# Performance work log

Hardware: AMD Instinct MI355X
Metric: run time of the kernel (lower is better)

Reference implementation:

```python
import jax, jax.numpy as jnp
import numpy as np

B, T1, CHUNK = 4, 512, 64
LEFT, RIGHT = 256, 64
T2 = T1 + LEFT + RIGHT          # 832
NPOS = 2 * T1 - 1 + LEFT + RIGHT  # 1343
NFEAT, H, DK = 1024, 16, 64


def setup_inputs() -> dict:
    key = jax.random.key(0)
    ks = jax.random.split(key, 14)
    s = 0.02
    inp = {
        "query":   jax.random.normal(ks[0], (B, T1, NFEAT), jnp.float32),
        "key":     jax.random.normal(ks[1], (B, T2, NFEAT), jnp.float32),
        "value":   jax.random.normal(ks[2], (B, T2, NFEAT), jnp.float32),
        "pos_emb": jax.random.normal(ks[3], (1, NPOS, NFEAT), jnp.float32),
        "Wq":   jax.random.normal(ks[4], (NFEAT, NFEAT), jnp.float32) * s,
        "bq":   jax.random.normal(ks[5], (NFEAT,), jnp.float32) * s,
        "Wk":   jax.random.normal(ks[6], (NFEAT, NFEAT), jnp.float32) * s,
        "bk":   jax.random.normal(ks[7], (NFEAT,), jnp.float32) * s,
        "Wv":   jax.random.normal(ks[8], (NFEAT, NFEAT), jnp.float32) * s,
        "bv":   jax.random.normal(ks[9], (NFEAT,), jnp.float32) * s,
        "Wpos": jax.random.normal(ks[10], (NFEAT, NFEAT), jnp.float32) * s,
        "Wout": jax.random.normal(ks[11], (NFEAT, NFEAT), jnp.float32) * s,
        "bout": jax.random.normal(ks[12], (NFEAT,), jnp.float32) * s,
        "pos_bias_u": jax.random.normal(ks[13], (H, DK), jnp.float32) * s,
        "pos_bias_v": jax.random.normal(jax.random.fold_in(key, 99), (H, DK), jnp.float32) * s,
    }
    # chunk mask with right context: key index j maps to absolute position a = j - LEFT;
    # query i (chunk c = i // CHUNK) may attend a in [c*CHUNK - LEFT, (c+1)*CHUNK + RIGHT)
    c = np.arange(T1) // CHUNK
    a = np.arange(T2) - LEFT
    allowed = (a[None, :] < (c[:, None] + 1) * CHUNK + RIGHT) & (a[None, :] >= c[:, None] * CHUNK - LEFT)
    inp["mask"] = jnp.broadcast_to(jnp.asarray(allowed, dtype=bool)[None], (B, T1, T2))
    inp["left_context_size"] = LEFT
    inp["right_context_size"] = RIGHT
    return inp


def _rel_shift(x, left, right):
    # x: (b, h, t1, 2*t1-1+left+right) -> (b, h, t1, t1+left+right)
    # matches torch as_strided: out[..., i, j] = x[..., i, j - i + t1 - 1]
    b, h, t1, n = x.shape
    t2 = t1 + left + right
    idx = jnp.arange(t2)[None, :] - jnp.arange(t1)[:, None] + (t1 - 1)  # (t1, t2)
    return jnp.take_along_axis(x, idx[None, None], axis=-1)


def reference(query, key, value, pos_emb, mask, Wq, bq, Wk, bk, Wv, bv,
              Wpos, Wout, bout, pos_bias_u, pos_bias_v,
              left_context_size, right_context_size):
    b, t1, _ = query.shape
    q = (query @ Wq.T + bq).reshape(b, t1, H, DK)                       # (b, t1, h, d)
    k = (key @ Wk.T + bk).reshape(b, -1, H, DK).transpose(0, 2, 1, 3)    # (b, h, t2, d)
    v = (value @ Wv.T + bv).reshape(b, -1, H, DK).transpose(0, 2, 1, 3)  # (b, h, t2, d)
    p = (pos_emb @ Wpos.T).reshape(pos_emb.shape[0], -1, H, DK).transpose(0, 2, 1, 3)  # (1, h, n, d)

    q_u = (q + pos_bias_u).transpose(0, 2, 1, 3)   # (b, h, t1, d)
    q_v = (q + pos_bias_v).transpose(0, 2, 1, 3)   # (b, h, t1, d)

    matrix_ac = jnp.einsum('bhqd,bhkd->bhqk', q_u, k)          # (b, h, t1, t2)
    matrix_bd = jnp.einsum('bhqd,ohnd->bhqn', q_v, p)          # (b, h, t1, n)
    matrix_bd = _rel_shift(matrix_bd, left_context_size, right_context_size)

    scores = (matrix_ac + matrix_bd) / jnp.sqrt(jnp.float32(DK))
    m = mask[:, None, :, :]                                    # (b, 1, t1, t2), True = attend
    scores = jnp.where(m, scores, -jnp.inf)
    attn = jax.nn.softmax(scores.astype(jnp.float32), axis=-1).astype(value.dtype)
    attn = jnp.where(m, attn, 0.0)

    x = jnp.einsum('bhqk,bhkd->bqhd', attn, v).reshape(b, t1, H * DK)
    out = x @ Wout.T + bout                                     # (b, t1, n_feat)
    new_cache = jnp.concatenate([k, v], axis=-1)                # (b, h, t2, 2*d)
    return out, new_cache
```

## Files before the change

kernel.cpp:

```cpp
#include <hip/hip_runtime.h>
#include <cstdint>

typedef unsigned short u16;
using short8 = __attribute__((ext_vector_type(8))) short;
using f32x4  = __attribute__((ext_vector_type(4))) float;

#define T1 512
#define T2 832
#define NH 16
#define NPLOC 448

__device__ __forceinline__ u16 f2b(float f){
  union { float f; uint32_t u; } c; c.f = f;
  uint32_t u = c.u;
  u += 0x7fffu + ((u >> 16) & 1u);
  return (u16)(u >> 16);
}
__device__ __forceinline__ float b2f(u16 b){
  union { uint32_t u; float f; } c; c.u = (uint32_t)b << 16; return c.f;
}
__device__ __forceinline__ void async16(const void* g, void* l){
  __builtin_amdgcn_global_load_lds(
      (const __attribute__((address_space(1))) unsigned int*)g,
      (__attribute__((address_space(3))) unsigned int*)l, 16, 0, 0);
}

#define SB0 __builtin_amdgcn_sched_barrier(0)

struct CvtSeg { const float* src; u16* dst; int nblk; };
struct CvtArgs { CvtSeg s[9]; };

__global__ __launch_bounds__(256) void cvt_all(CvtArgs a){
  int rel = blockIdx.x, seg = 0;
  while (rel >= a.s[seg].nblk){ rel -= a.s[seg].nblk; ++seg; }
  int i = rel * 256 + threadIdx.x;
  float4 v = ((const float4*)a.s[seg].src)[i];
  uint64_t p = (uint64_t)f2b(v.x) | ((uint64_t)f2b(v.y) << 16)
             | ((uint64_t)f2b(v.z) << 32) | ((uint64_t)f2b(v.w) << 48);
  *(uint64_t*)(a.s[seg].dst + (size_t)i * 4) = p;
}

struct G4Args {
  const u16 *q, *k, *v, *p;
  const u16 *Wq, *Wk, *Wv, *Wp;
  const float *bq, *bk, *bv, *pbu, *pbv;
  u16 *qu, *qv2, *katt, *vatt, *patt;
  float *cache;
};

__global__ __launch_bounds__(256, 2) void gemm4(G4Args ga){
  __shared__ __align__(16) u16 As0[8192];
  __shared__ __align__(16) u16 As1[8192];
  __shared__ __align__(16) u16 Bs0[8192];
  __shared__ __align__(16) u16 Bs1[8192];

  int bid0 = blockIdx.x;
  int bid = (bid0 & 7) * 72 + (bid0 >> 3);
  int tid = threadIdx.x;
  int mode, mb; const u16 *A, *W;
  if (bid < 128)      { mode = 0; mb = bid >> 3;         A = ga.q; W = ga.Wq; }
  else if (bid < 336) { mode = 1; mb = (bid - 128) >> 3; A = ga.k; W = ga.Wk; }
  else if (bid < 544) { mode = 2; mb = (bid - 336) >> 3; A = ga.v; W = ga.Wv; }
  else                { mode = 3; mb = (bid - 544) >> 3; A = ga.p; W = ga.Wp; }
  int m0 = mb * 128, n0 = (bid & 7) * 128;

  int lane = tid & 63, w = tid >> 6;
  int wr = w >> 1, wc = w & 1;
  const int lr = lane & 15, g = lane >> 4;
  const int r7 = lr & 7;

  int srow = tid >> 3;
  int ssl = ((tid & 7) ^ (srow & 7)) * 8;
  const u16* Asrc = A + (size_t)(m0 + srow) * 1024 + ssl;
  const u16* Bsrc = W + (size_t)(n0 + srow) * 1024 + ssl;

  f32x4 acc[4][4] = {};

  auto stage = [&](int k0, u16* as, u16* bs){
    #pragma unroll
    for (int cc = 0; cc < 4; ++cc){
      async16(Asrc + (size_t)cc*32768 + k0, as + cc*2048 + tid*8);
      async16(Bsrc + (size_t)cc*32768 + k0, bs + cc*2048 + tid*8);
    }
  };

  auto step = [&](u16* as, u16* bs, int kstage, bool do_stage, bool last){
    if (last) asm volatile("s_waitcnt vmcnt(0)" ::: "memory");
    else      asm volatile("s_waitcnt vmcnt(8)" ::: "memory");
    SB0; __builtin_amdgcn_s_barrier(); SB0;
    short8 a[2][4], b[2][4];
    #pragma unroll
    for (int kk = 0; kk < 2; ++kk){
      int sl = ((kk*4 + g) ^ r7) * 8;
      #pragma unroll
      for (int m = 0; m < 4; ++m) a[kk][m] = *(const short8*)&as[(wr*64 + m*16 + lr)*64 + sl];
      #pragma unroll
      for (int n = 0; n < 4; ++n) b[kk][n] = *(const short8*)&bs[(wc*64 + n*16 + lr)*64 + sl];
    }
    asm volatile("s_waitcnt lgkmcnt(0)" ::: "memory");
    SB0; __builtin_amdgcn_s_barrier(); SB0;
    if (do_stage) stage(kstage, as, bs);
    SB0;
    __builtin_amdgcn_s_setprio(1);
    #pragma unroll
    for (int kk = 0; kk < 2; ++kk)
      #pragma unroll
      for (int m = 0; m < 4; ++m)
        #pragma unroll
        for (int n = 0; n < 4; ++n)
          acc[m][n] = __builtin_amdgcn_mfma_f32_16x16x32_bf16(a[kk][m], b[kk][n], acc[m][n], 0, 0, 0);
    __builtin_amdgcn_s_setprio(0);
  };

  stage(0,  As0, Bs0);
  stage(64, As1, Bs1);
  SB0;
  for (int it = 0; it < 8; ++it){
    step(As0, Bs0, it*128 + 128, it < 7, false);
    step(As1, Bs1, it*128 + 192, it < 7, it == 7);
  }

  #pragma unroll
  for (int m = 0; m < 4; ++m){
    #pragma unroll
    for (int n = 0; n < 4; ++n){
      #pragma unroll
      for (int j = 0; j < 4; ++j){
        int row = m0 + wr*64 + m*16 + g*4 + j;
        int col = n0 + wc*64 + n*16 + lr;
        float vv = acc[m][n][j];
        if (mode == 0){
          vv += ga.bq[col];
          int h = col >> 6, d = col & 63, b_ = row >> 9, t = row & 511;
          size_t o = ((size_t)((b_*NH + h)*T1 + t))*64 + d;
          ga.qu [o] = f2b(vv + ga.pbu[col]);
          ga.qv2[o] = f2b(vv + ga.pbv[col]);
        } else if (mode == 1 || mode == 2){
          vv += (mode == 1 ? ga.bk : ga.bv)[col];
          int h = col >> 6, d = col & 63;
          int b_ = row / T2, t2 = row - b_*T2;
          size_t base = (size_t)(b_*NH + h)*T2 + t2;
          ga.cache[base*128 + (mode == 2 ? 64 : 0) + d] = vv;
          (mode == 1 ? ga.katt : ga.vatt)[base*64 + d] = f2b(vv);
        } else {
          if (row < NPLOC){
            int h = col >> 6, d = col & 63;
            ga.patt[((size_t)h*NPLOC + row)*64 + d] = f2b(vv);
          }
        }
      }
    }
  }
}

__device__ __forceinline__ void gemm_core64(const u16* __restrict__ A, const u16* __restrict__ W,
    int m0, int n0, int tid, f32x4 acc[4][2])
{
  __shared__ __align__(16) u16 As0[2048];
  __shared__ __align__(16) u16 As1[2048];
  __shared__ __align__(16) u16 Bs0[4096];
  __shared__ __align__(16) u16 Bs1[4096];

  int lane = tid & 63, wc = tid >> 6;
  const int lr = lane & 15, g = lane >> 4;
  const int sslot = (g ^ ((lr >> 1) & 3)) * 8;

  int r = tid >> 2;
  int ssl = ((tid & 3) ^ ((tid >> 3) & 3)) * 8;
  const u16* Asrc = A + (size_t)(m0 + r) * 1024 + ssl;
  const u16* Bsrc = W + (size_t)(n0 + r) * 1024 + ssl;

  auto stage = [&](int k0, u16* as, u16* bs){
    async16(Asrc + k0,         as + tid*8);
    async16(Bsrc + k0,         bs + tid*8);
    async16(Bsrc + 65536 + k0, bs + 2048 + tid*8);
  };

  auto step = [&](u16* as, u16* bs, int kstage, bool do_stage, bool last){
    if (last) asm volatile("s_waitcnt vmcnt(0)" ::: "memory");
    else      asm volatile("s_waitcnt vmcnt(3)" ::: "memory");
    SB0; __builtin_amdgcn_s_barrier(); SB0;
    short8 a[4], b[2];
    #pragma unroll
    for (int m = 0; m < 4; ++m) a[m] = *(const short8*)&as[(m*16 + lr)*32 + sslot];
    #pragma unroll
    for (int n = 0; n < 2; ++n) b[n] = *(const short8*)&bs[(wc*32 + n*16 + lr)*32 + sslot];
    asm volatile("s_waitcnt lgkmcnt(0)" ::: "memory");
    SB0; __builtin_amdgcn_s_barrier(); SB0;
    if (do_stage) stage(kstage, as, bs);
    SB0;
    __builtin_amdgcn_s_setprio(1);
    #pragma unroll
    for (int m = 0; m < 4; ++m)
      #pragma unroll
      for (int n = 0; n < 2; ++n)
        acc[m][n] = __builtin_amdgcn_mfma_f32_16x16x32_bf16(a[m], b[n], acc[m][n], 0, 0, 0);
    __builtin_amdgcn_s_setprio(0);
  };

  stage(0,  As0, Bs0);
  stage(32, As1, Bs1);
  SB0;
  for (int it = 0; it < 16; ++it){
    step(As0, Bs0, it*64 + 64, it < 15, false);
    step(As1, Bs1, it*64 + 96, it < 15, it == 15);
  }
}

__global__ __launch_bounds__(256, 4) void gemm_out(const u16* __restrict__ A, const u16* __restrict__ W,
                                                   const float* __restrict__ bias, float* __restrict__ out){
  int bid0 = blockIdx.x;
  int bid = (bid0 & 7) * 32 + (bid0 >> 3);
  int m0 = (bid >> 3) * 64, n0 = (bid & 7) * 128;
  int tid = threadIdx.x;
  f32x4 acc[4][2] = {};
  gemm_core64(A, W, m0, n0, tid, acc);
  int lane = tid & 63, wc = tid >> 6;
  const int lr = lane & 15, g = lane >> 4;
  #pragma unroll
  for (int m = 0; m < 4; ++m)
    #pragma unroll
    for (int n = 0; n < 2; ++n)
      #pragma unroll
      for (int j = 0; j < 4; ++j){
        int row = m0 + m*16 + g*4 + j;
        int col = n0 + wc*32 + n*16 + lr;
        out[(size_t)row*1024 + col] = acc[m][n][j] + bias[col];
      }
}

#define PHASE_HEAD(N) \
  asm volatile("s_waitcnt vmcnt(" #N ")" ::: "memory"); \
  SB0; __builtin_amdgcn_s_barrier(); SB0;

#define PHASE_TAIL \
  SB0; __builtin_amdgcn_s_barrier(); SB0;

#define VT_TAIL \
  asm volatile("s_waitcnt lgkmcnt(0)" ::: "memory"); \
  SB0; __builtin_amdgcn_s_barrier(); SB0;

__global__ __launch_bounds__(256, 2) void attn_v3(
    const u16* __restrict__ qu, const u16* __restrict__ qv,
    const u16* __restrict__ katt, const u16* __restrict__ vatt,
    const u16* __restrict__ patt, u16* __restrict__ xout)
{
  __shared__ __align__(16) u16 SB[64*384];
  __shared__ __align__(16) u16 S0[8192];
  __shared__ __align__(16) u16 S1[8192];

  int tid = threadIdx.x, lane = tid & 63, w = tid >> 6;
  int bid0 = blockIdx.x;
  int bid = (bid0 & 7) * 64 + (bid0 >> 3);
  int c = bid & 7, h = (bid >> 3) & 15, b = bid >> 7;
  int bh = b*NH + h;
  const int lr = lane & 15, g = lane >> 4, lk = g * 8;

  auto sb_off = [&](int r, int cc) -> uint32_t {
    return ((uint32_t)(r*384 + cc)*2) ^ ((uint32_t)(r & 15) << 4);
  };
  auto stg_swz = [&](uint32_t o) -> uint32_t { return o ^ (((o >> 7) & 7u) << 4); };
  auto vt_off = [&](int d, int kk) -> uint32_t {
    return ((uint32_t)(d*128 + kk)*2) ^ ((uint32_t)(((d & 7) ^ ((d >> 3) & 7))) << 4);
  };

  int qrow = 16*w + lr;
  const u16* qub = qu + ((size_t)bh*T1 + c*64 + qrow)*64;
  const u16* qvb = qv + ((size_t)bh*T1 + c*64 + qrow)*64;
  short8 qu0 = *(const short8*)(qub + lk);
  short8 qu1 = *(const short8*)(qub + 32 + lk);
  short8 qv0 = *(const short8*)(qvb + lk);
  short8 qv1 = *(const short8*)(qvb + 32 + lk);
  SB0;

  const char* psrc = (const char*)(patt + (size_t)h*NPLOC*64);
  const char* ksrc = (const char*)(katt + ((size_t)bh*T2 + c*64)*64);
  const u16*  vsrc = vatt + ((size_t)bh*T2 + c*64)*64;

  auto issue4 = [&](const char* src, u16* dst){
    #pragma unroll
    for (int i = 0; i < 4; ++i){
      uint32_t o = (uint32_t)(i*256 + tid)*16;
      async16(src + stg_swz(o), (char*)dst + o);
    }
  };

  uint4 vstg0, vstg1, vstg2, vstg3;
  auto vload = [&](int vc){
    const u16* vb = vsrc + vc*8192;
    vstg0 = *(const uint4*)(vb + (0*256 + tid)*8);
    vstg1 = *(const uint4*)(vb + (1*256 + tid)*8);
    vstg2 = *(const uint4*)(vb + (2*256 + tid)*8);
    vstg3 = *(const uint4*)(vb + (3*256 + tid)*8);
  };
  auto vtwrite = [&](u16* sbuf){
    #pragma unroll
    for (int i = 0; i < 4; ++i){
      uint4 vv4 = (i == 0) ? vstg0 : (i == 1) ? vstg1 : (i == 2) ? vstg2 : vstg3;
      int e = (i*256 + tid)*8;
      int kk = e >> 6, d0 = e & 63;
      u16 uu[8] = { (u16)(vv4.x & 0xffff), (u16)(vv4.x >> 16), (u16)(vv4.y & 0xffff), (u16)(vv4.y >> 16),
                    (u16)(vv4.z & 0xffff), (u16)(vv4.z >> 16), (u16)(vv4.w & 0xffff), (u16)(vv4.w >> 16) };
      #pragma unroll
      for (int j = 0; j < 8; ++j)
        *(u16*)((char*)sbuf + vt_off(d0 + j, kk)) = uu[j];
    }
  };

  #define BD_CHUNK(PC, SBUF) \
    _Pragma("unroll") \
    for (int nt = 0; nt < 8; ++nt){ \
      uint32_t bo = (uint32_t)((nt*16 + lr)*64)*2; \
      short8 b0 = *(const short8*)((const char*)SBUF + stg_swz(bo + lk*2)); \
      short8 b1 = *(const short8*)((const char*)SBUF + stg_swz(bo + (32 + lk)*2)); \
      f32x4 acc = {0.f,0.f,0.f,0.f}; \
      __builtin_amdgcn_s_setprio(1); \
      acc = __builtin_amdgcn_mfma_f32_16x16x32_bf16(qv0, b0, acc, 0, 0, 0); \
      acc = __builtin_amdgcn_mfma_f32_16x16x32_bf16(qv1, b1, acc, 0, 0, 0); \
      __builtin_amdgcn_s_setprio(0); \
      int nl = (PC)*128 + nt*16 + lr; \
      _Pragma("unroll") \
      for (int j = 0; j < 4; ++j){ \
        int r = 16*w + g*4 + j; \
        int jj = nl + r - 63; \
        if (jj >= 0 && jj < 384) *(u16*)((char*)SB + sb_off(r, jj)) = f2b(acc[j]); \
      } \
    }

  #define AC_CHUNK(KC, SBUF) \
    _Pragma("unroll") \
    for (int nt = 0; nt < 8; ++nt){ \
      uint32_t bo = (uint32_t)((nt*16 + lr)*64)*2; \
      short8 b0 = *(const short8*)((const char*)SBUF + stg_swz(bo + lk*2)); \
      short8 b1 = *(const short8*)((const char*)SBUF + stg_swz(bo + (32 + lk)*2)); \
      __builtin_amdgcn_s_setprio(1); \
      accs[(KC)*8 + nt] = __builtin_amdgcn_mfma_f32_16x16x32_bf16(qu0, b0, accs[(KC)*8 + nt], 0, 0, 0); \
      accs[(KC)*8 + nt] = __builtin_amdgcn_mfma_f32_16x16x32_bf16(qu1, b1, accs[(KC)*8 + nt], 0, 0, 0); \
      __builtin_amdgcn_s_setprio(0); \
    }

  #define PV_CHUNK(VC, SBUF) \
    _Pragma("unroll") \
    for (int kt = 0; kt < 4; ++kt){ \
      short8 a = *(const short8*)((const char*)SB + sb_off(16*w + lr, (VC)*128 + kt*32 + lk)); \
      __builtin_amdgcn_s_setprio(1); \
      _Pragma("unroll") \
      for (int n = 0; n < 4; ++n){ \
        short8 bb = *(const short8*)((const char*)SBUF + vt_off(n*16 + lr, kt*32 + lk)); \
        acco[n] = __builtin_amdgcn_mfma_f32_16x16x32_bf16(a, bb, acco[n], 0, 0, 0); \
      } \
      __builtin_amdgcn_s_setprio(0); \
    }

  f32x4 accs[24];
  #pragma unroll
  for (int t = 0; t < 24; ++t) accs[t] = (f32x4){0.f,0.f,0.f,0.f};
  f32x4 acco[4] = {};

  issue4(psrc,          S0);
  issue4(psrc + 16384,  S1);

  PHASE_HEAD(4) BD_CHUNK(0, S0) PHASE_TAIL issue4(psrc + 32768, S0);
  PHASE_HEAD(4) BD_CHUNK(1, S1) PHASE_TAIL issue4(psrc + 49152, S1);
  PHASE_HEAD(4) BD_CHUNK(2, S0) PHASE_TAIL issue4(ksrc,         S0);
  PHASE_HEAD(4) BD_CHUNK(3, S1) PHASE_TAIL issue4(ksrc + 16384, S1);
  PHASE_HEAD(4) AC_CHUNK(0, S0) PHASE_TAIL issue4(ksrc + 32768, S0);
  PHASE_HEAD(4) AC_CHUNK(1, S1) PHASE_TAIL vload(0);
  PHASE_HEAD(4) AC_CHUNK(2, S0)

  #pragma unroll
  for (int t = 0; t < 24; ++t)
    #pragma unroll
    for (int j = 0; j < 4; ++j){
      int r = 16*w + g*4 + j, cc = t*16 + lr;
      accs[t][j] += b2f(*(const u16*)((const char*)SB + sb_off(r, cc)));
    }
  float mx[4] = {-1e30f,-1e30f,-1e30f,-1e30f};
  #pragma unroll
  for (int t = 0; t < 24; ++t)
    #pragma unroll
    for (int j = 0; j < 4; ++j) mx[j] = fmaxf(mx[j], accs[t][j]);
  #pragma unroll
  for (int j = 0; j < 4; ++j){
    mx[j] = fmaxf(mx[j], __shfl_xor(mx[j], 1));
    mx[j] = fmaxf(mx[j], __shfl_xor(mx[j], 2));
    mx[j] = fmaxf(mx[j], __shfl_xor(mx[j], 4));
    mx[j] = fmaxf(mx[j], __shfl_xor(mx[j], 8));
  }
  float sm[4] = {0.f,0.f,0.f,0.f};
  #pragma unroll
  for (int t = 0; t < 24; ++t)
    #pragma unroll
    for (int j = 0; j < 4; ++j){
      accs[t][j] = __expf((accs[t][j] - mx[j]) * 0.125f);
      sm[j] += accs[t][j];
    }
  #pragma unroll
  for (int j = 0; j < 4; ++j){
    sm[j] += __shfl_xor(sm[j], 1);
    sm[j] += __shfl_xor(sm[j], 2);
    sm[j] += __shfl_xor(sm[j], 4);
    sm[j] += __shfl_xor(sm[j], 8);
    sm[j] = 1.f / sm[j];
  }
  #pragma unroll
  for (int t = 0; t < 24; ++t)
    #pragma unroll
    for (int j = 0; j < 4; ++j){
      int r = 16*w + g*4 + j, cc = t*16 + lr;
      *(u16*)((char*)SB + sb_off(r, cc)) = f2b(accs[t][j] * sm[j]);
    }

  asm volatile("s_waitcnt vmcnt(0)" ::: "memory");
  SB0;
  vtwrite(S1);
  vload(1);
  VT_TAIL

  PV_CHUNK(0, S1)
  asm volatile("s_waitcnt vmcnt(0)" ::: "memory");
  SB0;
  vtwrite(S0);
  vload(2);
  VT_TAIL

  PV_CHUNK(1, S0)
  asm volatile("s_waitcnt vmcnt(0)" ::: "memory");
  SB0;
  vtwrite(S1);
  VT_TAIL

  PV_CHUNK(2, S1)

  #pragma unroll
  for (int n = 0; n < 4; ++n)
    #pragma unroll
    for (int j = 0; j < 4; ++j){
      int r = 16*w + g*4 + j;
      int t = c*64 + r, d = n*16 + lr;
      xout[((size_t)b*T1 + t)*1024 + h*64 + d] = f2b(acco[n][j]);
    }
}

extern "C" void kernel_launch(void* const* d_in, const int* in_sizes, int n_in,
                              void* d_out, int out_size, void* d_ws, size_t ws_size,
                              hipStream_t stream)
{
  const float* query = (const float*)d_in[0];
  const float* key   = (const float*)d_in[1];
  const float* value = (const float*)d_in[2];
  const float* pos   = (const float*)d_in[3];
  const float* Wq  = (const float*)d_in[4];
  const float* bq  = (const float*)d_in[5];
  const float* Wk  = (const float*)d_in[6];
  const float* bk  = (const float*)d_in[7];
  const float* Wv  = (const float*)d_in[8];
  const float* bv  = (const float*)d_in[9];
  const float* Wp  = (const float*)d_in[10];
  const float* Wo  = (const float*)d_in[11];
  const float* bo  = (const float*)d_in[12];
  const float* pbu = (const float*)d_in[13];
  const float* pbv = (const float*)d_in[14];

  float* out   = (float*)d_out;
  float* cache = out + 2097152;

  u16* ws     = (u16*)d_ws;
  u16* q_bf   = ws;
  u16* key_bf = ws + 2097152;
  u16* val_bf = ws + 5505024;
  u16* pos_bf = ws + 8912896;
  u16* Wq_bf  = ws + 9437184;
  u16* Wk_bf  = ws + 10485760;
  u16* Wv_bf  = ws + 11534336;
  u16* Wp_bf  = ws + 12582912;
  u16* Wo_bf  = ws + 13631488;
  u16* qu_bf  = ws + 14680064;
  u16* qv_bf  = ws + 16777216;
  u16* katt   = ws + 18874368;
  u16* vatt   = ws + 22282240;
  u16* patt   = ws + 25690112;
  u16* x_bf   = ws + 26148864;

  CvtArgs ca;
  ca.s[0] = { query,            q_bf,   2048 };
  ca.s[1] = { key,              key_bf, 3328 };
  ca.s[2] = { value,            val_bf, 3328 };
  ca.s[3] = { Wq,               Wq_bf,  1024 };
  ca.s[4] = { Wk,               Wk_bf,  1024 };
  ca.s[5] = { Wv,               Wv_bf,  1024 };
  ca.s[6] = { Wp,               Wp_bf,  1024 };
  ca.s[7] = { Wo,               Wo_bf,  1024 };
  ca.s[8] = { pos + 448*1024,   pos_bf, 448 };
  cvt_all<<<14272, 256, 0, stream>>>(ca);

  G4Args ga;
  ga.q = q_bf; ga.k = key_bf; ga.v = val_bf; ga.p = pos_bf;
  ga.Wq = Wq_bf; ga.Wk = Wk_bf; ga.Wv = Wv_bf; ga.Wp = Wp_bf;
  ga.bq = bq; ga.bk = bk; ga.bv = bv; ga.pbu = pbu; ga.pbv = pbv;
  ga.qu = qu_bf; ga.qv2 = qv_bf; ga.katt = katt; ga.vatt = vatt; ga.patt = patt;
  ga.cache = cache;
  gemm4<<<576, 256, 0, stream>>>(ga);

  attn_v3<<<512, 256, 0, stream>>>(qu_bf, qv_bf, katt, vatt, patt, x_bf);

  gemm_out<<<256, 256, 0, stream>>>(x_bf, Wo_bf, bo, out);
}
```

Measured before the change: 99.07 us.

## Fuse fp32-to-bf16 activation conversion into projection GEMM A-tile loads

Activations (query, key, value, pos) are no longer pre-converted by cvt_all. The projection GEMM now async-loads fp32 A tiles into LDS and packs them to bf16 in registers just before the MFMAs. This removes a full write and read of the bf16 activation copies. In exchange the K tile shrinks from 64 to 32, so there are twice as many pipeline steps and barriers, and occupancy is raised to 3 blocks to fit the smaller LDS footprint.

```diff
diff --git a/kernel.cpp b/kernel.cpp
--- a/kernel.cpp
+++ b/kernel.cpp
@@ -1,4 +1,5 @@
 #include <hip/hip_runtime.h>
+#include <hip/hip_bf16.h>
 #include <cstdint>
 
 typedef unsigned short u16;
@@ -24,11 +25,21 @@
       (const __attribute__((address_space(1))) unsigned int*)g,
       (__attribute__((address_space(3))) unsigned int*)l, 16, 0, 0);
 }
+__device__ __forceinline__ short8 pk8(float4 fa, float4 fb){
+  union { __hip_bfloat162 h; uint32_t u; } c0, c1, c2, c3;
+  c0.h = __float22bfloat162_rn(make_float2(fa.x, fa.y));
+  c1.h = __float22bfloat162_rn(make_float2(fa.z, fa.w));
+  c2.h = __float22bfloat162_rn(make_float2(fb.x, fb.y));
+  c3.h = __float22bfloat162_rn(make_float2(fb.z, fb.w));
+  union { uint32_t u[4]; short8 s; } r;
+  r.u[0] = c0.u; r.u[1] = c1.u; r.u[2] = c2.u; r.u[3] = c3.u;
+  return r.s;
+}
 
 #define SB0 __builtin_amdgcn_sched_barrier(0)
 
 struct CvtSeg { const float* src; u16* dst; int nblk; };
-struct CvtArgs { CvtSeg s[9]; };
+struct CvtArgs { CvtSeg s[5]; };
 
 __global__ __launch_bounds__(256) void cvt_all(CvtArgs a){
   int rel = blockIdx.x, seg = 0;
@@ -41,23 +52,23 @@
 }
 
 struct G4Args {
-  const u16 *q, *k, *v, *p;
+  const float *q, *k, *v, *p;
   const u16 *Wq, *Wk, *Wv, *Wp;
   const float *bq, *bk, *bv, *pbu, *pbv;
   u16 *qu, *qv2, *katt, *vatt, *patt;
   float *cache;
 };
 
-__global__ __launch_bounds__(256, 2) void gemm4(G4Args ga){
-  __shared__ __align__(16) u16 As0[8192];
-  __shared__ __align__(16) u16 As1[8192];
-  __shared__ __align__(16) u16 Bs0[8192];
-  __shared__ __align__(16) u16 Bs1[8192];
+__global__ __launch_bounds__(256, 3) void gemm4(G4Args ga){
+  __shared__ __align__(16) float As0[4096];
+  __shared__ __align__(16) float As1[4096];
+  __shared__ __align__(16) u16   Bs0[4096];
+  __shared__ __align__(16) u16   Bs1[4096];
 
   int bid0 = blockIdx.x;
   int bid = (bid0 & 7) * 72 + (bid0 >> 3);
   int tid = threadIdx.x;
-  int mode, mb; const u16 *A, *W;
+  int mode, mb; const float *A; const u16 *W;
   if (bid < 128)      { mode = 0; mb = bid >> 3;         A = ga.q; W = ga.Wq; }
   else if (bid < 336) { mode = 1; mb = (bid - 128) >> 3; A = ga.k; W = ga.Wk; }
   else if (bid < 544) { mode = 2; mb = (bid - 336) >> 3; A = ga.v; W = ga.Wv; }
@@ -67,57 +78,60 @@
   int lane = tid & 63, w = tid >> 6;
   int wr = w >> 1, wc = w & 1;
   const int lr = lane & 15, g = lane >> 4;
+  const int sslot = (g ^ ((lr >> 1) & 3)) * 8;
   const int r7 = lr & 7;
 
-  int srow = tid >> 3;
-  int ssl = ((tid & 7) ^ (srow & 7)) * 8;
-  const u16* Asrc = A + (size_t)(m0 + srow) * 1024 + ssl;
-  const u16* Bsrc = W + (size_t)(n0 + srow) * 1024 + ssl;
+  const float* Af = A + (size_t)(m0 + (tid >> 3)) * 1024 + ((tid & 7) ^ ((tid >> 3) & 7)) * 4;
+  const u16* Bsrc = W + (size_t)(n0 + (tid >> 2)) * 1024 + ((tid & 3) ^ ((tid >> 3) & 3)) * 8;
 
   f32x4 acc[4][4] = {};
 
-  auto stage = [&](int k0, u16* as, u16* bs){
-    #pragma unroll
-    for (int cc = 0; cc < 4; ++cc){
-      async16(Asrc + (size_t)cc*32768 + k0, as + cc*2048 + tid*8);
-      async16(Bsrc + (size_t)cc*32768 + k0, bs + cc*2048 + tid*8);
-    }
-  };
-
-  auto step = [&](u16* as, u16* bs, int kstage, bool do_stage, bool last){
+  auto stage = [&](int kt, float* as, u16* bs){
+    #pragma unroll
+    for (int cc = 0; cc < 4; ++cc)
+      async16(Af + kt*32 + cc*32768, (char*)as + cc*4096 + tid*16);
+    async16(Bsrc + kt*32,         bs + tid*8);
+    async16(Bsrc + kt*32 + 65536, bs + 2048 + tid*8);
+  };
+
+  auto step = [&](float* as, u16* bs, int kstage, bool do_stage, bool last){
     if (last) asm volatile("s_waitcnt vmcnt(0)" ::: "memory");
-    else      asm volatile("s_waitcnt vmcnt(8)" ::: "memory");
+    else      asm volatile("s_waitcnt vmcnt(6)" ::: "memory");
     SB0; __builtin_amdgcn_s_barrier(); SB0;
-    short8 a[2][4], b[2][4];
-    #pragma unroll
-    for (int kk = 0; kk < 2; ++kk){
-      int sl = ((kk*4 + g) ^ r7) * 8;
-      #pragma unroll
-      for (int m = 0; m < 4; ++m) a[kk][m] = *(const short8*)&as[(wr*64 + m*16 + lr)*64 + sl];
-      #pragma unroll
-      for (int n = 0; n < 4; ++n) b[kk][n] = *(const short8*)&bs[(wc*64 + n*16 + lr)*64 + sl];
-    }
+    const char* ab = (const char*)as;
+    float4 fa[4], fb[4];
+    short8 b[4];
+    #pragma unroll
+    for (int m = 0; m < 4; ++m){
+      int rr = wr*64 + m*16 + lr;
+      int s0 = (g*2) ^ r7;
+      fa[m] = *(const float4*)(ab + rr*128 + s0*16);
+      fb[m] = *(const float4*)(ab + rr*128 + (s0^1)*16);
+    }
+    #pragma unroll
+    for (int n = 0; n < 4; ++n) b[n] = *(const short8*)&bs[(wc*64 + n*16 + lr)*32 + sslot];
     asm volatile("s_waitcnt lgkmcnt(0)" ::: "memory");
     SB0; __builtin_amdgcn_s_barrier(); SB0;
     if (do_stage) stage(kstage, as, bs);
     SB0;
+    short8 a[4];
+    #pragma unroll
+    for (int m = 0; m < 4; ++m) a[m] = pk8(fa[m], fb[m]);
     __builtin_amdgcn_s_setprio(1);
     #pragma unroll
-    for (int kk = 0; kk < 2; ++kk)
+    for (int m = 0; m < 4; ++m)
       #pragma unroll
-      for (int m = 0; m < 4; ++m)
-        #pragma unroll
-        for (int n = 0; n < 4; ++n)
-          acc[m][n] = __builtin_amdgcn_mfma_f32_16x16x32_bf16(a[kk][m], b[kk][n], acc[m][n], 0, 0, 0);
+      for (int n = 0; n < 4; ++n)
+        acc[m][n] = __builtin_amdgcn_mfma_f32_16x16x32_bf16(a[m], b[n], acc[m][n], 0, 0, 0);
     __builtin_amdgcn_s_setprio(0);
   };
 
-  stage(0,  As0, Bs0);
-  stage(64, As1, Bs1);
+  stage(0, As0, Bs0);
+  stage(1, As1, Bs1);
   SB0;
-  for (int it = 0; it < 8; ++it){
-    step(As0, Bs0, it*128 + 128, it < 7, false);
-    step(As1, Bs1, it*128 + 192, it < 7, it == 7);
+  for (int it = 0; it < 16; ++it){
+    step(As0, Bs0, 2*it + 2, it < 15, false);
+    step(As1, Bs1, 2*it + 3, it < 15, it == 15);
   }
 
   #pragma unroll
@@ -466,10 +480,6 @@
   float* cache = out + 2097152;
 
   u16* ws     = (u16*)d_ws;
-  u16* q_bf   = ws;
-  u16* key_bf = ws + 2097152;
-  u16* val_bf = ws + 5505024;
-  u16* pos_bf = ws + 8912896;
   u16* Wq_bf  = ws + 9437184;
   u16* Wk_bf  = ws + 10485760;
   u16* Wv_bf  = ws + 11534336;
@@ -483,19 +493,15 @@
   u16* x_bf   = ws + 26148864;
 
   CvtArgs ca;
-  ca.s[0] = { query,            q_bf,   2048 };
-  ca.s[1] = { key,              key_bf, 3328 };
-  ca.s[2] = { value,            val_bf, 3328 };
-  ca.s[3] = { Wq,               Wq_bf,  1024 };
-  ca.s[4] = { Wk,               Wk_bf,  1024 };
-  ca.s[5] = { Wv,               Wv_bf,  1024 };
-  ca.s[6] = { Wp,               Wp_bf,  1024 };
-  ca.s[7] = { Wo,               Wo_bf,  1024 };
-  ca.s[8] = { pos + 448*1024,   pos_bf, 448 };
-  cvt_all<<<14272, 256, 0, stream>>>(ca);
+  ca.s[0] = { Wq, Wq_bf, 1024 };
+  ca.s[1] = { Wk, Wk_bf, 1024 };
+  ca.s[2] = { Wv, Wv_bf, 1024 };
+  ca.s[3] = { Wp, Wp_bf, 1024 };
+  ca.s[4] = { Wo, Wo_bf, 1024 };
+  cvt_all<<<5120, 256, 0, stream>>>(ca);
 
   G4Args ga;
-  ga.q = q_bf; ga.k = key_bf; ga.v = val_bf; ga.p = pos_bf;
+  ga.q = query; ga.k = key; ga.v = value; ga.p = pos + 448*1024;
   ga.Wq = Wq_bf; ga.Wk = Wk_bf; ga.Wv = Wv_bf; ga.Wp = Wp_bf;
   ga.bq = bq; ga.bk = bk; ga.bv = bv; ga.pbu = pbu; ga.pbv = pbv;
   ga.qu = qu_bf; ga.qv2 = qv_bf; ga.katt = katt; ga.vatt = vatt; ga.patt = patt;
```

Result: faster. 91.26 us (-7.9%).

## Halve gemm4 K-tile for higher occupancy and move pos-bias add into attention

Applied to the files above, without the earlier changes.

The projection GEMM now stages 32-wide K slices instead of 64-wide, halving shared memory per block so launch bounds can allow 4 blocks per CU. The main loop runs twice as many iterations with half the loads per stage. Separately, the Q projection writes a single bf16 Q tensor, and the attention kernel adds pos_bias_u/v itself on load. This removes one Q store and one Q load stream. The trade-offs are more barriers per K, double bf16 rounding on q+bias, and lower register headroom.

```diff
diff --git a/kernel.cpp b/kernel.cpp
--- a/kernel.cpp
+++ b/kernel.cpp
@@ -23,6 +23,12 @@
   __builtin_amdgcn_global_load_lds(
       (const __attribute__((address_space(1))) unsigned int*)g,
       (__attribute__((address_space(3))) unsigned int*)l, 16, 0, 0);
+}
+__device__ __forceinline__ short8 addbias(short8 q, const float* bp){
+  short8 r;
+  #pragma unroll
+  for (int j = 0; j < 8; ++j) r[j] = (short)f2b(b2f((u16)q[j]) + bp[j]);
+  return r;
 }
 
 #define SB0 __builtin_amdgcn_sched_barrier(0)
@@ -43,16 +49,16 @@
 struct G4Args {
   const u16 *q, *k, *v, *p;
   const u16 *Wq, *Wk, *Wv, *Wp;
-  const float *bq, *bk, *bv, *pbu, *pbv;
-  u16 *qu, *qv2, *katt, *vatt, *patt;
+  const float *bq, *bk, *bv;
+  u16 *qatt, *katt, *vatt, *patt;
   float *cache;
 };
 
-__global__ __launch_bounds__(256, 2) void gemm4(G4Args ga){
-  __shared__ __align__(16) u16 As0[8192];
-  __shared__ __align__(16) u16 As1[8192];
-  __shared__ __align__(16) u16 Bs0[8192];
-  __shared__ __align__(16) u16 Bs1[8192];
+__global__ __launch_bounds__(256, 4) void gemm4(G4Args ga){
+  __shared__ __align__(16) u16 As0[4096];
+  __shared__ __align__(16) u16 As1[4096];
+  __shared__ __align__(16) u16 Bs0[4096];
+  __shared__ __align__(16) u16 Bs1[4096];
 
   int bid0 = blockIdx.x;
   int bid = (bid0 & 7) * 72 + (bid0 >> 3);
@@ -67,57 +73,50 @@
   int lane = tid & 63, w = tid >> 6;
   int wr = w >> 1, wc = w & 1;
   const int lr = lane & 15, g = lane >> 4;
-  const int r7 = lr & 7;
-
-  int srow = tid >> 3;
-  int ssl = ((tid & 7) ^ (srow & 7)) * 8;
-  const u16* Asrc = A + (size_t)(m0 + srow) * 1024 + ssl;
-  const u16* Bsrc = W + (size_t)(n0 + srow) * 1024 + ssl;
+  const int sslot = (g ^ ((lr >> 1) & 3)) * 8;
+
+  int r = tid >> 2;
+  int ssl = ((tid & 3) ^ ((tid >> 3) & 3)) * 8;
+  const u16* Asrc = A + (size_t)(m0 + r) * 1024 + ssl;
+  const u16* Bsrc = W + (size_t)(n0 + r) * 1024 + ssl;
 
   f32x4 acc[4][4] = {};
 
   auto stage = [&](int k0, u16* as, u16* bs){
-    #pragma unroll
-    for (int cc = 0; cc < 4; ++cc){
-      async16(Asrc + (size_t)cc*32768 + k0, as + cc*2048 + tid*8);
-      async16(Bsrc + (size_t)cc*32768 + k0, bs + cc*2048 + tid*8);
-    }
+    async16(Asrc + k0,         as + tid*8);
+    async16(Asrc + 65536 + k0, as + 2048 + tid*8);
+    async16(Bsrc + k0,         bs + tid*8);
+    async16(Bsrc + 65536 + k0, bs + 2048 + tid*8);
   };
 
   auto step = [&](u16* as, u16* bs, int kstage, bool do_stage, bool last){
     if (last) asm volatile("s_waitcnt vmcnt(0)" ::: "memory");
-    else      asm volatile("s_waitcnt vmcnt(8)" ::: "memory");
+    else      asm volatile("s_waitcnt vmcnt(4)" ::: "memory");
     SB0; __builtin_amdgcn_s_barrier(); SB0;
-    short8 a[2][4], b[2][4];
-    #pragma unroll
-    for (int kk = 0; kk < 2; ++kk){
-      int sl = ((kk*4 + g) ^ r7) * 8;
-      #pragma unroll
-      for (int m = 0; m < 4; ++m) a[kk][m] = *(const short8*)&as[(wr*64 + m*16 + lr)*64 + sl];
-      #pragma unroll
-      for (int n = 0; n < 4; ++n) b[kk][n] = *(const short8*)&bs[(wc*64 + n*16 + lr)*64 + sl];
-    }
+    short8 a[4], b[4];
+    #pragma unroll
+    for (int m = 0; m < 4; ++m) a[m] = *(const short8*)&as[(wr*64 + m*16 + lr)*32 + sslot];
+    #pragma unroll
+    for (int n = 0; n < 4; ++n) b[n] = *(const short8*)&bs[(wc*64 + n*16 + lr)*32 + sslot];
     asm volatile("s_waitcnt lgkmcnt(0)" ::: "memory");
     SB0; __builtin_amdgcn_s_barrier(); SB0;
     if (do_stage) stage(kstage, as, bs);
     SB0;
     __builtin_amdgcn_s_setprio(1);
     #pragma unroll
-    for (int kk = 0; kk < 2; ++kk)
+    for (int m = 0; m < 4; ++m)
       #pragma unroll
-      for (int m = 0; m < 4; ++m)
-        #pragma unroll
-        for (int n = 0; n < 4; ++n)
-          acc[m][n] = __builtin_amdgcn_mfma_f32_16x16x32_bf16(a[kk][m], b[kk][n], acc[m][n], 0, 0, 0);
+      for (int n = 0; n < 4; ++n)
+        acc[m][n] = __builtin_amdgcn_mfma_f32_16x16x32_bf16(a[m], b[n], acc[m][n], 0, 0, 0);
     __builtin_amdgcn_s_setprio(0);
   };
 
   stage(0,  As0, Bs0);
-  stage(64, As1, Bs1);
+  stage(32, As1, Bs1);
   SB0;
-  for (int it = 0; it < 8; ++it){
-    step(As0, Bs0, it*128 + 128, it < 7, false);
-    step(As1, Bs1, it*128 + 192, it < 7, it == 7);
+  for (int it = 0; it < 16; ++it){
+    step(As0, Bs0, it*64 + 64, it < 15, false);
+    step(As1, Bs1, it*64 + 96, it < 15, it == 15);
   }
 
   #pragma unroll
@@ -133,8 +132,7 @@
           vv += ga.bq[col];
           int h = col >> 6, d = col & 63, b_ = row >> 9, t = row & 511;
           size_t o = ((size_t)((b_*NH + h)*T1 + t))*64 + d;
-          ga.qu [o] = f2b(vv + ga.pbu[col]);
-          ga.qv2[o] = f2b(vv + ga.pbv[col]);
+          ga.qatt[o] = f2b(vv);
         } else if (mode == 1 || mode == 2){
           vv += (mode == 1 ? ga.bk : ga.bv)[col];
           int h = col >> 6, d = col & 63;
@@ -241,9 +239,11 @@
   SB0; __builtin_amdgcn_s_barrier(); SB0;
 
 __global__ __launch_bounds__(256, 2) void attn_v3(
-    const u16* __restrict__ qu, const u16* __restrict__ qv,
+    const u16* __restrict__ qatt,
     const u16* __restrict__ katt, const u16* __restrict__ vatt,
-    const u16* __restrict__ patt, u16* __restrict__ xout)
+    const u16* __restrict__ patt,
+    const float* __restrict__ pbu, const float* __restrict__ pbv,
+    u16* __restrict__ xout)
 {
   __shared__ __align__(16) u16 SB[64*384];
   __shared__ __align__(16) u16 S0[8192];
@@ -265,12 +265,15 @@
   };
 
   int qrow = 16*w + lr;
-  const u16* qub = qu + ((size_t)bh*T1 + c*64 + qrow)*64;
-  const u16* qvb = qv + ((size_t)bh*T1 + c*64 + qrow)*64;
-  short8 qu0 = *(const short8*)(qub + lk);
-  short8 qu1 = *(const short8*)(qub + 32 + lk);
-  short8 qv0 = *(const short8*)(qvb + lk);
-  short8 qv1 = *(const short8*)(qvb + 32 + lk);
+  const u16* qb = qatt + ((size_t)bh*T1 + c*64 + qrow)*64;
+  short8 q0 = *(const short8*)(qb + lk);
+  short8 q1 = *(const short8*)(qb + 32 + lk);
+  const float* bu = pbu + h*64;
+  const float* bv = pbv + h*64;
+  short8 qu0 = addbias(q0, bu + lk);
+  short8 qu1 = addbias(q1, bu + 32 + lk);
+  short8 qv0 = addbias(q0, bv + lk);
+  short8 qv1 = addbias(q1, bv + 32 + lk);
   SB0;
 
   const char* psrc = (const char*)(patt + (size_t)h*NPLOC*64);
@@ -475,8 +478,7 @@
   u16* Wv_bf  = ws + 11534336;
   u16* Wp_bf  = ws + 12582912;
   u16* Wo_bf  = ws + 13631488;
-  u16* qu_bf  = ws + 14680064;
-  u16* qv_bf  = ws + 16777216;
+  u16* qatt   = ws + 14680064;
   u16* katt   = ws + 18874368;
   u16* vatt   = ws + 22282240;
   u16* patt   = ws + 25690112;
@@ -497,12 +499,12 @@
   G4Args ga;
   ga.q = q_bf; ga.k = key_bf; ga.v = val_bf; ga.p = pos_bf;
   ga.Wq = Wq_bf; ga.Wk = Wk_bf; ga.Wv = Wv_bf; ga.Wp = Wp_bf;
-  ga.bq = bq; ga.bk = bk; ga.bv = bv; ga.pbu = pbu; ga.pbv = pbv;
-  ga.qu = qu_bf; ga.qv2 = qv_bf; ga.katt = katt; ga.vatt = vatt; ga.patt = patt;
+  ga.bq = bq; ga.bk = bk; ga.bv = bv;
+  ga.qatt = qatt; ga.katt = katt; ga.vatt = vatt; ga.patt = patt;
   ga.cache = cache;
   gemm4<<<576, 256, 0, stream>>>(ga);
 
-  attn_v3<<<512, 256, 0, stream>>>(qu_bf, qv_bf, katt, vatt, patt, x_bf);
+  attn_v3<<<512, 256, 0, stream>>>(qatt, katt, vatt, patt, pbu, pbv, x_bf);
 
   gemm_out<<<256, 256, 0, stream>>>(x_bf, Wo_bf, bo, out);
 }
```

Measured after the change: 90.30 us. -8.8%, faster.
